# Performance work log

Measured on AMD Instinct MI355X. Metric: run time of the kernel, lower is better.

## Reference

```python
import jax, jax.numpy as jnp
import numpy as np

DIM = 512
HEADS = 8
HD = DIM // HEADS          # head_dim = 64
GROUPS = 32                # GroupNorm groups
EPS = 1e-5
SCALE = HD ** -0.25        # double-scale: applied to both q and k
B, H, W, L, CTX = 8, 32, 32, 77, 768


def setup_inputs() -> dict:
    key = jax.random.key(0)
    ks = jax.random.split(key, 6)
    return {
        "x": jax.random.normal(ks[0], (B, DIM, H, W), jnp.float32),
        "context": jax.random.normal(ks[1], (B, L, CTX), jnp.float32),
        "gn_gamma": jnp.ones((DIM,), jnp.float32),
        "gn_beta": jnp.zeros((DIM,), jnp.float32),
        "qkv_w": jax.random.normal(ks[2], (3 * DIM, DIM), jnp.float32) * 0.02,
        "qkv_b": jnp.zeros((3 * DIM,), jnp.float32),
        "ckv_w": jax.random.normal(ks[3], (2 * DIM, CTX), jnp.float32) * 0.02,
        "ckv_b": jnp.zeros((2 * DIM,), jnp.float32),
        "proj_w": jax.random.normal(ks[4], (DIM, DIM), jnp.float32) * 0.02,
        "proj_b": jnp.zeros((DIM,), jnp.float32),
    }


def _group_norm(x, gamma, beta):
    b, c, h, w = x.shape
    xr = x.reshape(b, GROUPS, c // GROUPS, h, w)
    mu = xr.mean(axis=(2, 3, 4), keepdims=True)
    var = xr.var(axis=(2, 3, 4), keepdims=True)
    xr = (xr - mu) * jax.lax.rsqrt(var + EPS)
    return xr.reshape(b, c, h, w) * gamma[None, :, None, None] + beta[None, :, None, None]


def reference(x, context, gn_gamma, gn_beta, qkv_w, qkv_b, ckv_w, ckv_b, proj_w, proj_b):
    b, c, h, w = x.shape
    n, d = HEADS, HD
    identity = x

    xn = _group_norm(x, gn_gamma, gn_beta)
    # 1x1 conv == channel GEMM. qkv: [b, 3*dim, h*w] -> [b, 3, n, d, hw]
    qkv = jnp.einsum('bchw,oc->bohw', xn, qkv_w) + qkv_b[None, :, None, None]
    qkv = qkv.reshape(b, 3, n, d, h * w)
    q, k, v = qkv[:, 0], qkv[:, 1], qkv[:, 2]   # each [b, n, d, hw]

    # context kv: Linear(context_dim, 2*dim) -> [b, L, 2, n, d] -> [b, n, d, L]
    ckv = jnp.einsum('blc,oc->blo', context, ckv_w) + ckv_b
    ckv = ckv.reshape(b, -1, 2, n, d)
    ck = jnp.transpose(ckv[:, :, 0], (0, 2, 3, 1))  # [b, n, d, L]
    cv = jnp.transpose(ckv[:, :, 1], (0, 2, 3, 1))
    k = jnp.concatenate([ck, k], axis=-1)           # [b, n, d, L+hw]
    v = jnp.concatenate([cv, v], axis=-1)

    # attn = (q^T * s) @ (k * s); softmax over keys
    attn = jnp.einsum('bndq,bndk->bnqk', q * SCALE, k * SCALE)
    attn = jax.nn.softmax(attn, axis=-1)
    out = jnp.einsum('bndk,bnqk->bndq', v, attn).reshape(b, c, h, w)

    out = jnp.einsum('bchw,oc->bohw', out, proj_w) + proj_b[None, :, None, None]
    return out + identity
```

## Files before the change

kernel.cpp:

```cpp
#include <hip/hip_runtime.h>

#define B_ 8
#define DIM_ 512
#define HEADS_ 8
#define HD_ 64
#define HW_ 1024
#define L_ 77
#define LP_ 80
#define CTX_ 768
#define KV_ 1101
#define KVP_ 1152
#define NPAD_ 51
#define CTX0_ 1024
#define SC_QK 0.42466089f

typedef __attribute__((ext_vector_type(8))) short bf16x8;
typedef __attribute__((ext_vector_type(4))) float f32x4;
typedef __attribute__((ext_vector_type(4))) unsigned short u16x4;

__device__ __forceinline__ unsigned short f2bf(float f) {
  union { float f; unsigned int u; } c; c.f = f;
  unsigned int u = c.u;
  return (unsigned short)((u + 0x7fffu + ((u >> 16) & 1u)) >> 16);
}
__device__ __forceinline__ float bf2f(unsigned short h) {
  union { unsigned int u; float f; } c; c.u = ((unsigned int)h) << 16;
  return c.f;
}

#define GLD_LDS16(gsrc, ldst) \
  __builtin_amdgcn_global_load_lds((const __attribute__((address_space(1))) void*)(gsrc), \
                                   (__attribute__((address_space(3))) void*)(ldst), 16, 0, 0)

__global__ __launch_bounds__(256) void prep_k(const float* __restrict__ x,
                                              const float* __restrict__ gamma,
                                              const float* __restrict__ beta,
                                              const float* __restrict__ qkv_w,
                                              const float* __restrict__ ckv_w,
                                              const float* __restrict__ proj_w,
                                              const float* __restrict__ ctx,
                                              unsigned short* __restrict__ xn_t,
                                              unsigned short* __restrict__ dq,
                                              unsigned short* __restrict__ dc,
                                              unsigned short* __restrict__ dp,
                                              unsigned short* __restrict__ ctx_bf,
                                              unsigned short* __restrict__ k_s,
                                              unsigned short* __restrict__ vT) {
  __shared__ unsigned short xs[16][1032];
  __shared__ float red[8];
  int bid = blockIdx.x;
  int tid = threadIdx.x;
  if (bid < 256) {
    const int b = bid >> 5, g = bid & 31;
    const float* xp = x + ((size_t)b * DIM_ + g * 16) * HW_;
    float sum = 0.f, ssq = 0.f;
#pragma unroll
    for (int i = 0; i < 16; ++i) {
      float4 v = *(const float4*)&xp[i * HW_ + tid * 4];
      sum += v.x + v.y + v.z + v.w;
      ssq += v.x * v.x + v.y * v.y + v.z * v.z + v.w * v.w;
      xs[i][tid * 4 + 0] = f2bf(v.x);
      xs[i][tid * 4 + 1] = f2bf(v.y);
      xs[i][tid * 4 + 2] = f2bf(v.z);
      xs[i][tid * 4 + 3] = f2bf(v.w);
    }
#pragma unroll
    for (int off = 32; off >= 1; off >>= 1) {
      sum += __shfl_xor(sum, off, 64);
      ssq += __shfl_xor(ssq, off, 64);
    }
    if ((tid & 63) == 0) { red[(tid >> 6) * 2] = sum; red[(tid >> 6) * 2 + 1] = ssq; }
    __syncthreads();
    sum = red[0] + red[2] + red[4] + red[6];
    ssq = red[1] + red[3] + red[5] + red[7];
    float mu = sum * (1.f / 16384.f);
    float rstd = rsqrtf(ssq * (1.f / 16384.f) - mu * mu + 1e-5f);
    float a[16], c[16];
#pragma unroll
    for (int ci = 0; ci < 16; ++ci) {
      float gm = gamma[g * 16 + ci], bt = beta[g * 16 + ci];
      a[ci] = rstd * gm;
      c[ci] = bt - mu * rstd * gm;
    }
#pragma unroll
    for (int t = 0; t < 4; ++t) {
      int hw = tid + t * 256;
      unsigned short tmp[16];
#pragma unroll
      for (int ci = 0; ci < 16; ++ci)
        tmp[ci] = f2bf(bf2f(xs[ci][hw]) * a[ci] + c[ci]);
      unsigned int w[8];
#pragma unroll
      for (int j = 0; j < 8; ++j) w[j] = (unsigned int)tmp[2 * j] | ((unsigned int)tmp[2 * j + 1] << 16);
      unsigned short* dptr = &xn_t[((size_t)b * HW_ + hw) * DIM_ + g * 16];
      *(uint4*)dptr = make_uint4(w[0], w[1], w[2], w[3]);
      *(uint4*)(dptr + 8) = make_uint4(w[4], w[5], w[6], w[7]);
    }
  } else if (bid < 2048) {
    int i = (bid - 256) * 256 + tid;
    const float* src;
    unsigned short* dst;
    int off;
    if (i < 196608) { src = qkv_w; dst = dq; off = i; }
    else if (i < 393216) { src = ckv_w; dst = dc; off = i - 196608; }
    else { src = proj_w; dst = dp; off = i - 393216; }
    float4 v = *(const float4*)(src + (size_t)off * 4);
    u16x4 o;
    o[0] = f2bf(v.x); o[1] = f2bf(v.y); o[2] = f2bf(v.z); o[3] = f2bf(v.w);
    *(u16x4*)(dst + (size_t)off * 4) = o;
  } else if (bid < 2528) {
    int i = (bid - 2048) * 256 + tid;
    int idx = i * 4;
    int b = idx / (LP_ * CTX_);
    int rem = idx - b * (LP_ * CTX_);
    int l = rem / CTX_;
    int c = rem - l * CTX_;
    float4 v = make_float4(0.f, 0.f, 0.f, 0.f);
    if (l < L_) v = *(const float4*)&ctx[((size_t)b * L_ + l) * CTX_ + c];
    u16x4 o;
    o[0] = f2bf(v.x); o[1] = f2bf(v.y); o[2] = f2bf(v.z); o[3] = f2bf(v.w);
    *(u16x4*)(ctx_bf + idx) = o;
  } else {
    int i = (bid - 2528) * 256 + tid;
    int bh = i / (NPAD_ * 64);
    int rem = i - bh * (NPAD_ * 64);
    int row = KV_ + rem / 64;
    int d = rem & 63;
    k_s[((size_t)bh * KVP_ + row) * HD_ + d] = 0;
    vT[((size_t)bh * HD_ + d) * KVP_ + row] = 0;
  }
}

template <int MODE, int BM, int BN>
__device__ __forceinline__ void gemm_body(int bid,
                                          const unsigned short* __restrict__ A,
                                          const unsigned short* __restrict__ Bt,
                                          int M, int N, int K,
                                          const float* __restrict__ bias,
                                          unsigned short* __restrict__ out_q,
                                          unsigned short* __restrict__ out_k,
                                          unsigned short* __restrict__ out_v,
                                          const float* __restrict__ xres,
                                          float* __restrict__ outf,
                                          unsigned short* sm) {
  constexpr int MR = BM / 32;
  constexpr int NR = BN / 32;
  constexpr int AG = BM / 64;
  constexpr int BG = BN / 64;
  constexpr int SLOADS = AG + BG;
  unsigned short* As0 = sm;
  unsigned short* Bs0 = sm + 3 * BM * 32;
  const int tid = threadIdx.x;
  const int wid = tid >> 6, lane = tid & 63;
  const int lr = lane & 15, lg = lane >> 4;
  const int ntn = N / BN;
  const int tm = bid / ntn, tn = bid - tm * ntn;
  const int m0 = tm * BM, n0 = tn * BN;
  const int wr = wid >> 1, wc = wid & 1;
  f32x4 acc[MR][NR] = {};
  const int nkt = K >> 5;

  auto stage = [&](int bi, int kk) {
#pragma unroll
    for (int i = 0; i < AG; ++i) {
      int c = i * 256 + tid;
      int row = c >> 2, l = (c & 3) ^ ((row >> 1) & 3);
      GLD_LDS16(A + (size_t)(m0 + row) * K + kk + l * 8,
                As0 + (size_t)bi * BM * 32 + (size_t)c * 8);
    }
#pragma unroll
    for (int i = 0; i < BG; ++i) {
      int c = i * 256 + tid;
      int row = c >> 2, l = (c & 3) ^ ((row >> 1) & 3);
      GLD_LDS16(Bt + (size_t)(n0 + row) * K + kk + l * 8,
                Bs0 + (size_t)bi * BN * 32 + (size_t)c * 8);
    }
  };

  __builtin_amdgcn_sched_barrier(0);
  stage(0, 0);
  __builtin_amdgcn_sched_barrier(0);
  stage(1, 32);
  __builtin_amdgcn_sched_barrier(0);

  int cur = 0;
  for (int kt = 0; kt < nkt; ++kt) {
    if (kt < nkt - 1) {
      if constexpr (SLOADS == 4) asm volatile("s_waitcnt vmcnt(4)" ::: "memory");
      else                       asm volatile("s_waitcnt vmcnt(3)" ::: "memory");
    } else {
      asm volatile("s_waitcnt vmcnt(0)" ::: "memory");
    }
    __builtin_amdgcn_sched_barrier(0);
    __builtin_amdgcn_s_barrier();
    __builtin_amdgcn_sched_barrier(0);
    if (kt + 2 < nkt) stage(cur == 0 ? 2 : cur - 1, (kt + 2) << 5);
    const unsigned short* Ab = As0 + cur * BM * 32;
    const unsigned short* Bb = Bs0 + cur * BN * 32;
    bf16x8 af[MR], bf[NR];
#pragma unroll
    for (int mi = 0; mi < MR; ++mi) {
      int row = wr * (BM / 2) + mi * 16 + lr;
      af[mi] = *(const bf16x8*)&Ab[row * 32 + ((lg ^ ((row >> 1) & 3)) * 8)];
    }
#pragma unroll
    for (int nj = 0; nj < NR; ++nj) {
      int row = wc * (BN / 2) + nj * 16 + lr;
      bf[nj] = *(const bf16x8*)&Bb[row * 32 + ((lg ^ ((row >> 1) & 3)) * 8)];
    }
#pragma unroll
    for (int mi = 0; mi < MR; ++mi)
#pragma unroll
      for (int nj = 0; nj < NR; ++nj)
        acc[mi][nj] = __builtin_amdgcn_mfma_f32_16x16x32_bf16(af[mi], bf[nj], acc[mi][nj], 0, 0, 0);
    cur = (cur == 2) ? 0 : cur + 1;
  }

  if constexpr (MODE == 0) {
    __syncthreads();
    const int which = n0 >> 9;
    const int bb = m0 >> 10;
    const int qibase = m0 & 1023;
    if (which == 2) {
      uint2* Vt = (uint2*)sm;
#pragma unroll
      for (int mi = 0; mi < MR; ++mi) {
#pragma unroll
        for (int nj = 0; nj < NR; ++nj) {
          int col = wc * 64 + nj * 16 + lr;
          float b = bias[n0 + col];
          unsigned int w0, w1;
          float v0 = acc[mi][nj][0] + b, v1 = acc[mi][nj][1] + b;
          float v2 = acc[mi][nj][2] + b, v3 = acc[mi][nj][3] + b;
          asm("v_cvt_pk_bf16_f32 %0, %1, %2" : "=v"(w0) : "v"(v0), "v"(v1));
          asm("v_cvt_pk_bf16_f32 %0, %1, %2" : "=v"(w1) : "v"(v2), "v"(v3));
          int chunk = (wr * 16 + mi * 4 + lg) ^ (lr * 2);
          Vt[col * 32 + chunk] = make_uint2(w0, w1);
        }
      }
      __syncthreads();
#pragma unroll
      for (int it = 0; it < 8; ++it) {
        int col = wid * 32 + it * 4 + lg;
        uint4 val = *(uint4*)&Vt[col * 32 + ((lr * 2) ^ ((col & 15) * 2))];
        int colg = n0 + col;
        int head = (colg >> 6) & 7, d = colg & 63;
        *(uint4*)&out_v[(((size_t)bb * HEADS_ + head) * HD_ + d) * KVP_ + qibase + lr * 8] = val;
      }
    } else {
      unsigned short* Tq = sm;
#pragma unroll
      for (int mi = 0; mi < MR; ++mi) {
#pragma unroll
        for (int nj = 0; nj < NR; ++nj) {
          int col = wc * 64 + nj * 16 + lr;
          float b = bias[n0 + col];
          int qr = wr * 64 + mi * 16 + lg * 4;
#pragma unroll
          for (int r = 0; r < 4; ++r)
            Tq[(qr + r) * 132 + col] = f2bf((acc[mi][nj][r] + b) * SC_QK);
        }
      }
      __syncthreads();
#pragma unroll
      for (int it = 0; it < 8; ++it) {
        int qi = wid * 32 + it * 4 + lg;
        uint2 lo = *(uint2*)&Tq[qi * 132 + lr * 8];
        uint2 hi = *(uint2*)&Tq[qi * 132 + lr * 8 + 4];
        uint4 val = make_uint4(lo.x, lo.y, hi.x, hi.y);
        int colg = n0 + lr * 8;
        int head = (colg >> 6) & 7, d = colg & 63;
        size_t bh = (size_t)bb * HEADS_ + head;
        if (which == 0)
          *(uint4*)&out_q[(bh * HW_ + qibase + qi) * HD_ + d] = val;
        else
          *(uint4*)&out_k[(bh * KVP_ + qibase + qi) * HD_ + d] = val;
      }
    }
  } else {
#pragma unroll
    for (int mi = 0; mi < MR; ++mi) {
#pragma unroll
      for (int nj = 0; nj < NR; ++nj) {
#pragma unroll
        for (int r = 0; r < 4; ++r) {
          int row = m0 + wr * (BM / 2) + mi * 16 + lg * 4 + r;
          int col = n0 + wc * (BN / 2) + nj * 16 + lr;
          float v = acc[mi][nj][r];
          if (MODE == 1) {
            int bb = row / LP_, l = row - bb * LP_;
            if (l < L_) {
              v += bias[col];
              int which = col >> 9, head = (col >> 6) & 7, d = col & 63;
              size_t bh = (size_t)bb * HEADS_ + head;
              if (which == 0) out_k[(bh * KVP_ + CTX0_ + l) * HD_ + d] = f2bf(v * SC_QK);
              else            out_v[(bh * HD_ + d) * KVP_ + CTX0_ + l] = f2bf(v);
            }
          } else {
            size_t idx = (size_t)(col >> 10) * (DIM_ * HW_) + (size_t)row * HW_ + (col & 1023);
            outf[idx] = v + bias[row] + xres[idx];
          }
        }
      }
    }
  }
}

__global__ __launch_bounds__(256, 3) void gemm_qkv_ckv_k(
    const unsigned short* __restrict__ xn_t, const unsigned short* __restrict__ qkvw,
    const unsigned short* __restrict__ ctx_bf, const unsigned short* __restrict__ ckvw,
    const float* __restrict__ qkv_b, const float* __restrict__ ckv_b,
    unsigned short* __restrict__ q_s, unsigned short* __restrict__ k_s,
    unsigned short* __restrict__ vT) {
  __shared__ unsigned short sm[3 * 256 * 32];
  int bid = blockIdx.x;
  if (bid < 80) {
    gemm_body<1, 64, 128>(bid, ctx_bf, ckvw, 640, 1024, 768, ckv_b,
                          nullptr, k_s, vT, nullptr, nullptr, sm);
  } else {
    int b = bid - 80;
    int b2 = (b & 7) * 96 + (b >> 3);
    gemm_body<0, 128, 128>(b2, xn_t, qkvw, 8192, 1536, 512, qkv_b,
                           q_s, k_s, vT, nullptr, nullptr, sm);
  }
}

__global__ __launch_bounds__(256, 4) void gemm_proj_k(
    const unsigned short* __restrict__ projw, const unsigned short* __restrict__ at_s,
    const float* __restrict__ proj_b, const float* __restrict__ x,
    float* __restrict__ out) {
  __shared__ unsigned short sm[3 * 192 * 32];
  gemm_body<2, 64, 128>(blockIdx.x, projw, at_s, 512, 8192, 512, proj_b,
                        nullptr, nullptr, nullptr, x, out, sm);
}

#define PSTRIDE 72

__device__ __forceinline__ void attn_tile64(const unsigned short* __restrict__ Ksb,
                                            const unsigned short* __restrict__ Vsb,
                                            const bf16x8 (&qf)[2][2], const bf16x8 ones,
                                            unsigned short* __restrict__ Pw0,
                                            unsigned short* __restrict__ Pw1,
                                            int lr, int lg,
                                            const int (&ro)[4], const int (&koff)[2],
                                            f32x4 (&lacc)[2], f32x4 (&acc)[2][4]) {
  f32x4 st[2][4] = {};
  __builtin_amdgcn_s_setprio(1);
#pragma unroll
  for (int ks = 0; ks < 2; ++ks) {
    bf16x8 kf[4];
#pragma unroll
    for (int t = 0; t < 4; ++t)
      kf[t] = *(const bf16x8*)&Ksb[ro[t] + koff[ks]];
#pragma unroll
    for (int t = 0; t < 4; ++t) {
      st[0][t] = __builtin_amdgcn_mfma_f32_16x16x32_bf16(kf[t], qf[0][ks], st[0][t], 0, 0, 0);
      st[1][t] = __builtin_amdgcn_mfma_f32_16x16x32_bf16(kf[t], qf[1][ks], st[1][t], 0, 0, 0);
    }
  }
  __builtin_amdgcn_s_setprio(0);
#pragma unroll
  for (int c = 0; c < 2; ++c) {
#pragma unroll
    for (int t = 0; t < 4; ++t)
#pragma unroll
      for (int r = 0; r < 4; ++r) st[c][t][r] = __builtin_amdgcn_exp2f(st[c][t][r]);
    unsigned short* Pw = c ? Pw1 : Pw0;
#pragma unroll
    for (int t = 0; t < 4; ++t) {
      unsigned int w0, w1;
      asm("v_cvt_pk_bf16_f32 %0, %1, %2" : "=v"(w0) : "v"(st[c][t][0]), "v"(st[c][t][1]));
      asm("v_cvt_pk_bf16_f32 %0, %1, %2" : "=v"(w1) : "v"(st[c][t][2]), "v"(st[c][t][3]));
      *(uint2*)&Pw[lr * PSTRIDE + t * 16 + lg * 4] = make_uint2(w0, w1);
    }
  }
#pragma unroll
  for (int ks = 0; ks < 2; ++ks) {
    bf16x8 pb0 = *(const bf16x8*)&Pw0[lr * PSTRIDE + ks * 32 + lg * 8];
    bf16x8 pb1 = *(const bf16x8*)&Pw1[lr * PSTRIDE + ks * 32 + lg * 8];
    __builtin_amdgcn_s_setprio(1);
    lacc[0] = __builtin_amdgcn_mfma_f32_16x16x32_bf16(ones, pb0, lacc[0], 0, 0, 0);
    lacc[1] = __builtin_amdgcn_mfma_f32_16x16x32_bf16(ones, pb1, lacc[1], 0, 0, 0);
#pragma unroll
    for (int dt = 0; dt < 4; ++dt) {
      bf16x8 vf = *(const bf16x8*)&Vsb[ro[dt] + koff[ks]];
      acc[0][dt] = __builtin_amdgcn_mfma_f32_16x16x32_bf16(vf, pb0, acc[0][dt], 0, 0, 0);
      acc[1][dt] = __builtin_amdgcn_mfma_f32_16x16x32_bf16(vf, pb1, acc[1][dt], 0, 0, 0);
    }
    __builtin_amdgcn_s_setprio(0);
  }
}

__global__ __launch_bounds__(256, 3) void attn_k(const unsigned short* __restrict__ q_s,
                                                 const unsigned short* __restrict__ k_s,
                                                 const unsigned short* __restrict__ vT,
                                                 unsigned short* __restrict__ at_s) {
  __shared__ unsigned short Ks[2][4096];
  __shared__ unsigned short Vs[2][4096];
  __shared__ unsigned short Pb[4][2][16 * PSTRIDE];
  const int tid = threadIdx.x;
  const int wid = tid >> 6, lane = tid & 63;
  const int lr = lane & 15, lg = lane >> 4;
  const int bidx = blockIdx.x;
  const int xcd = bidx & 7, idx = bidx >> 3;
  const int bh = xcd + 8 * (idx >> 3);
  const int qt = idx & 7;
  const int q0 = qt * 128 + wid * 32;
  const unsigned short* qp = q_s + (size_t)bh * HW_ * HD_;
  const unsigned short* kp = k_s + (size_t)bh * KVP_ * HD_;
  const unsigned short* vp = vT + (size_t)bh * HD_ * KVP_;
  unsigned short* Pw0 = Pb[wid][0];
  unsigned short* Pw1 = Pb[wid][1];

  const int srow = lane >> 3;
  const int schunk = (lane & 7) ^ srow;

  auto stage = [&](int bufi, int kk) {
#pragma unroll
    for (int jj = 0; jj < 2; ++jj) {
      GLD_LDS16(kp + (size_t)(kk + wid * 16 + jj * 8 + srow) * HD_ + schunk * 8,
                &Ks[bufi][(wid * 2 + jj) * 512]);
      GLD_LDS16(vp + (size_t)(wid * 16 + jj * 8 + srow) * KVP_ + kk + schunk * 8,
                &Vs[bufi][(wid * 2 + jj) * 512]);
    }
  };

  int ro[4], koff[2];
#pragma unroll
  for (int t = 0; t < 4; ++t) ro[t] = (t * 16 + lr) * 64;
#pragma unroll
  for (int ks = 0; ks < 2; ++ks) koff[ks] = ((ks * 4 + lg) ^ (lr & 7)) * 8;

  bf16x8 qf[2][2];
#pragma unroll
  for (int c = 0; c < 2; ++c)
#pragma unroll
    for (int ks = 0; ks < 2; ++ks)
      qf[c][ks] = *(const bf16x8*)&qp[(size_t)(q0 + c * 16 + lr) * HD_ + ks * 32 + lg * 8];

  bf16x8 ones;
#pragma unroll
  for (int j = 0; j < 8; ++j) ones[j] = (short)0x3F80;

  f32x4 acc[2][4] = {};
  f32x4 lacc[2] = {};

  __builtin_amdgcn_sched_barrier(0);
  stage(0, 0);
  __builtin_amdgcn_sched_barrier(0);
  stage(1, 64);
  __builtin_amdgcn_sched_barrier(0);

  int cur = 0;
  for (int it = 0; it < 17; ++it) {
    asm volatile("s_waitcnt vmcnt(4)" ::: "memory");
    __builtin_amdgcn_sched_barrier(0);
    __builtin_amdgcn_s_barrier();
    __builtin_amdgcn_sched_barrier(0);
    attn_tile64(Ks[cur], Vs[cur], qf, ones, Pw0, Pw1, lr, lg, ro, koff, lacc, acc);
    asm volatile("s_waitcnt lgkmcnt(0)" ::: "memory");
    __builtin_amdgcn_sched_barrier(0);
    __builtin_amdgcn_s_barrier();
    __builtin_amdgcn_sched_barrier(0);
    if (it < 16) stage(cur, (it + 2) * 64);
    cur ^= 1;
  }
  asm volatile("s_waitcnt vmcnt(0)" ::: "memory");
  __builtin_amdgcn_sched_barrier(0);
  __builtin_amdgcn_s_barrier();
  __builtin_amdgcn_sched_barrier(0);
  attn_tile64(Ks[cur], Vs[cur], qf, ones, Pw0, Pw1, lr, lg, ro, koff, lacc, acc);

  const int bb = bh >> 3, head = bh & 7;
#pragma unroll
  for (int c = 0; c < 2; ++c) {
    const float inv = 1.f / (lacc[c][0] - (float)NPAD_);
    const int qi = q0 + c * 16 + lr;
#pragma unroll
    for (int dt = 0; dt < 4; ++dt) {
      u16x4 o;
#pragma unroll
      for (int r = 0; r < 4; ++r) o[r] = f2bf(acc[c][dt][r] * inv);
      *(u16x4*)&at_s[((size_t)bb * HW_ + qi) * DIM_ + head * HD_ + dt * 16 + lg * 4] = o;
    }
  }
}

extern "C" void kernel_launch(void* const* d_in, const int* in_sizes, int n_in,
                              void* d_out, int out_size, void* d_ws, size_t ws_size,
                              hipStream_t stream) {
  (void)in_sizes; (void)n_in; (void)out_size; (void)ws_size;
  const float* x      = (const float*)d_in[0];
  const float* ctx    = (const float*)d_in[1];
  const float* gng    = (const float*)d_in[2];
  const float* gnb    = (const float*)d_in[3];
  const float* qkv_w  = (const float*)d_in[4];
  const float* qkv_b  = (const float*)d_in[5];
  const float* ckv_w  = (const float*)d_in[6];
  const float* ckv_b  = (const float*)d_in[7];
  const float* proj_w = (const float*)d_in[8];
  const float* proj_b = (const float*)d_in[9];
  float* out = (float*)d_out;

  char* ws = (char*)d_ws;
  size_t off = 0;
  auto alloc = [&](size_t bytes) {
    char* p = ws + off;
    off = (off + bytes + 255) & ~(size_t)255;
    return p;
  };
  unsigned short* xn_t    = (unsigned short*)alloc((size_t)B_ * HW_ * DIM_ * 2);
  unsigned short* ctx_bf  = (unsigned short*)alloc((size_t)B_ * LP_ * CTX_ * 2);
  unsigned short* qkvw_bf = (unsigned short*)alloc((size_t)3 * DIM_ * DIM_ * 2);
  unsigned short* ckvw_bf = (unsigned short*)alloc((size_t)2 * DIM_ * CTX_ * 2);
  unsigned short* projw_bf= (unsigned short*)alloc((size_t)DIM_ * DIM_ * 2);
  unsigned short* q_s     = (unsigned short*)alloc((size_t)64 * HW_ * HD_ * 2);
  unsigned short* k_s     = (unsigned short*)alloc((size_t)64 * KVP_ * HD_ * 2);
  unsigned short* vT      = (unsigned short*)alloc((size_t)64 * HD_ * KVP_ * 2);
  unsigned short* at_s    = (unsigned short*)alloc((size_t)B_ * HW_ * DIM_ * 2);

  prep_k<<<3344, 256, 0, stream>>>(x, gng, gnb, qkv_w, ckv_w, proj_w, ctx,
                                   xn_t, qkvw_bf, ckvw_bf, projw_bf, ctx_bf, k_s, vT);
  gemm_qkv_ckv_k<<<848, 256, 0, stream>>>(xn_t, qkvw_bf, ctx_bf, ckvw_bf,
                                          qkv_b, ckv_b, q_s, k_s, vT);
  attn_k<<<512, 256, 0, stream>>>(q_s, k_s, vT, at_s);
  gemm_proj_k<<<512, 256, 0, stream>>>(projw_bf, at_s, proj_b, x, out);
}
```

Before: 75.52 us.

## Use 8 waves with 16 queries each and triple-buffered K/V in attention

Result: no change. 77.00 us (+2.0%).

```diff
diff --git a/kernel.cpp b/kernel.cpp
--- a/kernel.cpp
+++ b/kernel.cpp
@@ -338,13 +338,12 @@
 
 __device__ __forceinline__ void attn_tile64(const unsigned short* __restrict__ Ksb,
                                             const unsigned short* __restrict__ Vsb,
-                                            const bf16x8 (&qf)[2][2], const bf16x8 ones,
-                                            unsigned short* __restrict__ Pw0,
-                                            unsigned short* __restrict__ Pw1,
+                                            const bf16x8 (&qf)[2], const bf16x8 ones,
+                                            unsigned short* __restrict__ Pw,
                                             int lr, int lg,
                                             const int (&ro)[4], const int (&koff)[2],
-                                            f32x4 (&lacc)[2], f32x4 (&acc)[2][4]) {
-  f32x4 st[2][4] = {};
+                                            f32x4& lacc, f32x4 (&acc)[4]) {
+  f32x4 st[4] = {};
   __builtin_amdgcn_s_setprio(1);
 #pragma unroll
   for (int ks = 0; ks < 2; ++ks) {
@@ -353,51 +352,42 @@
     for (int t = 0; t < 4; ++t)
       kf[t] = *(const bf16x8*)&Ksb[ro[t] + koff[ks]];
 #pragma unroll
-    for (int t = 0; t < 4; ++t) {
-      st[0][t] = __builtin_amdgcn_mfma_f32_16x16x32_bf16(kf[t], qf[0][ks], st[0][t], 0, 0, 0);
-      st[1][t] = __builtin_amdgcn_mfma_f32_16x16x32_bf16(kf[t], qf[1][ks], st[1][t], 0, 0, 0);
-    }
+    for (int t = 0; t < 4; ++t)
+      st[t] = __builtin_amdgcn_mfma_f32_16x16x32_bf16(kf[t], qf[ks], st[t], 0, 0, 0);
   }
   __builtin_amdgcn_s_setprio(0);
 #pragma unroll
-  for (int c = 0; c < 2; ++c) {
-#pragma unroll
-    for (int t = 0; t < 4; ++t)
-#pragma unroll
-      for (int r = 0; r < 4; ++r) st[c][t][r] = __builtin_amdgcn_exp2f(st[c][t][r]);
-    unsigned short* Pw = c ? Pw1 : Pw0;
-#pragma unroll
-    for (int t = 0; t < 4; ++t) {
-      unsigned int w0, w1;
-      asm("v_cvt_pk_bf16_f32 %0, %1, %2" : "=v"(w0) : "v"(st[c][t][0]), "v"(st[c][t][1]));
-      asm("v_cvt_pk_bf16_f32 %0, %1, %2" : "=v"(w1) : "v"(st[c][t][2]), "v"(st[c][t][3]));
-      *(uint2*)&Pw[lr * PSTRIDE + t * 16 + lg * 4] = make_uint2(w0, w1);
-    }
+  for (int t = 0; t < 4; ++t)
+#pragma unroll
+    for (int r = 0; r < 4; ++r) st[t][r] = __builtin_amdgcn_exp2f(st[t][r]);
+#pragma unroll
+  for (int t = 0; t < 4; ++t) {
+    unsigned int w0, w1;
+    asm("v_cvt_pk_bf16_f32 %0, %1, %2" : "=v"(w0) : "v"(st[t][0]), "v"(st[t][1]));
+    asm("v_cvt_pk_bf16_f32 %0, %1, %2" : "=v"(w1) : "v"(st[t][2]), "v"(st[t][3]));
+    *(uint2*)&Pw[lr * PSTRIDE + t * 16 + lg * 4] = make_uint2(w0, w1);
   }
 #pragma unroll
   for (int ks = 0; ks < 2; ++ks) {
-    bf16x8 pb0 = *(const bf16x8*)&Pw0[lr * PSTRIDE + ks * 32 + lg * 8];
-    bf16x8 pb1 = *(const bf16x8*)&Pw1[lr * PSTRIDE + ks * 32 + lg * 8];
+    bf16x8 pb = *(const bf16x8*)&Pw[lr * PSTRIDE + ks * 32 + lg * 8];
     __builtin_amdgcn_s_setprio(1);
-    lacc[0] = __builtin_amdgcn_mfma_f32_16x16x32_bf16(ones, pb0, lacc[0], 0, 0, 0);
-    lacc[1] = __builtin_amdgcn_mfma_f32_16x16x32_bf16(ones, pb1, lacc[1], 0, 0, 0);
+    lacc = __builtin_amdgcn_mfma_f32_16x16x32_bf16(ones, pb, lacc, 0, 0, 0);
 #pragma unroll
     for (int dt = 0; dt < 4; ++dt) {
       bf16x8 vf = *(const bf16x8*)&Vsb[ro[dt] + koff[ks]];
-      acc[0][dt] = __builtin_amdgcn_mfma_f32_16x16x32_bf16(vf, pb0, acc[0][dt], 0, 0, 0);
-      acc[1][dt] = __builtin_amdgcn_mfma_f32_16x16x32_bf16(vf, pb1, acc[1][dt], 0, 0, 0);
+      acc[dt] = __builtin_amdgcn_mfma_f32_16x16x32_bf16(vf, pb, acc[dt], 0, 0, 0);
     }
     __builtin_amdgcn_s_setprio(0);
   }
 }
 
-__global__ __launch_bounds__(256, 3) void attn_k(const unsigned short* __restrict__ q_s,
+__global__ __launch_bounds__(512, 4) void attn_k(const unsigned short* __restrict__ q_s,
                                                  const unsigned short* __restrict__ k_s,
                                                  const unsigned short* __restrict__ vT,
                                                  unsigned short* __restrict__ at_s) {
-  __shared__ unsigned short Ks[2][4096];
-  __shared__ unsigned short Vs[2][4096];
-  __shared__ unsigned short Pb[4][2][16 * PSTRIDE];
+  __shared__ unsigned short Ks[3][4096];
+  __shared__ unsigned short Vs[3][4096];
+  __shared__ unsigned short Pb[8][16 * PSTRIDE];
   const int tid = threadIdx.x;
   const int wid = tid >> 6, lane = tid & 63;
   const int lr = lane & 15, lg = lane >> 4;
@@ -405,23 +395,26 @@
   const int xcd = bidx & 7, idx = bidx >> 3;
   const int bh = xcd + 8 * (idx >> 3);
   const int qt = idx & 7;
-  const int q0 = qt * 128 + wid * 32;
+  const int q0 = qt * 128 + wid * 16;
   const unsigned short* qp = q_s + (size_t)bh * HW_ * HD_;
   const unsigned short* kp = k_s + (size_t)bh * KVP_ * HD_;
   const unsigned short* vp = vT + (size_t)bh * HD_ * KVP_;
-  unsigned short* Pw0 = Pb[wid][0];
-  unsigned short* Pw1 = Pb[wid][1];
+  unsigned short* Pw = Pb[wid];
 
   const int srow = lane >> 3;
   const int schunk = (lane & 7) ^ srow;
 
   auto stage = [&](int bufi, int kk) {
-#pragma unroll
-    for (int jj = 0; jj < 2; ++jj) {
-      GLD_LDS16(kp + (size_t)(kk + wid * 16 + jj * 8 + srow) * HD_ + schunk * 8,
-                &Ks[bufi][(wid * 2 + jj) * 512]);
-      GLD_LDS16(vp + (size_t)(wid * 16 + jj * 8 + srow) * KVP_ + kk + schunk * 8,
-                &Vs[bufi][(wid * 2 + jj) * 512]);
+    if (wid < 4) {
+#pragma unroll
+      for (int jj = 0; jj < 2; ++jj)
+        GLD_LDS16(kp + (size_t)(kk + wid * 16 + jj * 8 + srow) * HD_ + schunk * 8,
+                  &Ks[bufi][(wid * 2 + jj) * 512]);
+    } else {
+#pragma unroll
+      for (int jj = 0; jj < 2; ++jj)
+        GLD_LDS16(vp + (size_t)((wid - 4) * 16 + jj * 8 + srow) * KVP_ + kk + schunk * 8,
+                  &Vs[bufi][((wid - 4) * 2 + jj) * 512]);
     }
   };
 
@@ -431,19 +424,17 @@
 #pragma unroll
   for (int ks = 0; ks < 2; ++ks) koff[ks] = ((ks * 4 + lg) ^ (lr & 7)) * 8;
 
-  bf16x8 qf[2][2];
-#pragma unroll
-  for (int c = 0; c < 2; ++c)
-#pragma unroll
-    for (int ks = 0; ks < 2; ++ks)
-      qf[c][ks] = *(const bf16x8*)&qp[(size_t)(q0 + c * 16 + lr) * HD_ + ks * 32 + lg * 8];
+  bf16x8 qf[2];
+#pragma unroll
+  for (int ks = 0; ks < 2; ++ks)
+    qf[ks] = *(const bf16x8*)&qp[(size_t)(q0 + lr) * HD_ + ks * 32 + lg * 8];
 
   bf16x8 ones;
 #pragma unroll
   for (int j = 0; j < 8; ++j) ones[j] = (short)0x3F80;
 
-  f32x4 acc[2][4] = {};
-  f32x4 lacc[2] = {};
+  f32x4 acc[4] = {};
+  f32x4 lacc = {};
 
   __builtin_amdgcn_sched_barrier(0);
   stage(0, 0);
@@ -451,38 +442,32 @@
   stage(1, 64);
   __builtin_amdgcn_sched_barrier(0);
 
-  int cur = 0;
-  for (int it = 0; it < 17; ++it) {
-    asm volatile("s_waitcnt vmcnt(4)" ::: "memory");
+  for (int it = 0; it < 18; ++it) {
+    if (it < 17) {
+      asm volatile("s_waitcnt vmcnt(2)" ::: "memory");
+    } else {
+      asm volatile("s_waitcnt vmcnt(0)" ::: "memory");
+    }
     __builtin_amdgcn_sched_barrier(0);
     __builtin_amdgcn_s_barrier();
     __builtin_amdgcn_sched_barrier(0);
-    attn_tile64(Ks[cur], Vs[cur], qf, ones, Pw0, Pw1, lr, lg, ro, koff, lacc, acc);
-    asm volatile("s_waitcnt lgkmcnt(0)" ::: "memory");
-    __builtin_amdgcn_sched_barrier(0);
-    __builtin_amdgcn_s_barrier();
-    __builtin_amdgcn_sched_barrier(0);
-    if (it < 16) stage(cur, (it + 2) * 64);
-    cur ^= 1;
-  }
-  asm volatile("s_waitcnt vmcnt(0)" ::: "memory");
-  __builtin_amdgcn_sched_barrier(0);
-  __builtin_amdgcn_s_barrier();
-  __builtin_amdgcn_sched_barrier(0);
-  attn_tile64(Ks[cur], Vs[cur], qf, ones, Pw0, Pw1, lr, lg, ro, koff, lacc, acc);
+    if (it + 2 < 18) {
+      int bi = it + 2;
+      stage(bi - (bi / 3) * 3, bi * 64);
+    }
+    int cb = it - (it / 3) * 3;
+    attn_tile64(Ks[cb], Vs[cb], qf, ones, Pw, lr, lg, ro, koff, lacc, acc);
+  }
 
   const int bb = bh >> 3, head = bh & 7;
-#pragma unroll
-  for (int c = 0; c < 2; ++c) {
-    const float inv = 1.f / (lacc[c][0] - (float)NPAD_);
-    const int qi = q0 + c * 16 + lr;
-#pragma unroll
-    for (int dt = 0; dt < 4; ++dt) {
-      u16x4 o;
-#pragma unroll
-      for (int r = 0; r < 4; ++r) o[r] = f2bf(acc[c][dt][r] * inv);
-      *(u16x4*)&at_s[((size_t)bb * HW_ + qi) * DIM_ + head * HD_ + dt * 16 + lg * 4] = o;
-    }
+  const float inv = 1.f / (lacc[0] - (float)NPAD_);
+  const int qi = q0 + lr;
+#pragma unroll
+  for (int dt = 0; dt < 4; ++dt) {
+    u16x4 o;
+#pragma unroll
+    for (int r = 0; r < 4; ++r) o[r] = f2bf(acc[dt][r] * inv);
+    *(u16x4*)&at_s[((size_t)bb * HW_ + qi) * DIM_ + head * HD_ + dt * 16 + lg * 4] = o;
   }
 }
 
@@ -523,6 +508,6 @@
                                    xn_t, qkvw_bf, ckvw_bf, projw_bf, ctx_bf, k_s, vT);
   gemm_qkv_ckv_k<<<848, 256, 0, stream>>>(xn_t, qkvw_bf, ctx_bf, ckvw_bf,
                                           qkv_b, ckv_b, q_s, k_s, vT);
-  attn_k<<<512, 256, 0, stream>>>(q_s, k_s, vT, at_s);
+  attn_k<<<512, 512, 0, stream>>>(q_s, k_s, vT, at_s);
   gemm_proj_k<<<512, 256, 0, stream>>>(projw_bf, at_s, proj_b, x, out);
 }
```
